# Optimization experiments

Measured on AMD Instinct MI355X. Metric: run time of the kernel, lower is better.

Reference implementation:

```python
import jax, jax.numpy as jnp
import numpy as np

N_NODES = 100000
NUM_ET = 8
IN_DIM = 128
N_EDGES = 100000


def setup_inputs() -> dict:
    key = jax.random.key(0)
    k1, k2, k3, k4 = jax.random.split(key, 4)
    z = jax.random.normal(k1, (N_NODES, IN_DIM), dtype=jnp.float32)
    # reset_parameters: normal with std = 1/sqrt(in_dim)
    weight = jax.random.normal(k2, (NUM_ET, IN_DIM), dtype=jnp.float32) / np.sqrt(IN_DIM)
    edge_src = jax.random.randint(k3, (NUM_ET, N_EDGES), 0, N_NODES, dtype=jnp.int64)
    edge_dst = jax.random.randint(k4, (NUM_ET, N_EDGES), 0, N_NODES, dtype=jnp.int64)
    return {"z": z, "weight": weight, "edge_src": edge_src, "edge_dst": edge_dst}


def reference(z, weight, edge_src, edge_dst):
    # For each edge type t and edge e: sigmoid( sum_d z[src,d] * z[dst,d] * weight[t,d] )
    zs = z[edge_src]                      # [T, E, D] gather
    zd = z[edge_dst]                      # [T, E, D] gather
    val = jnp.einsum('ted,ted,td->te', zs, zd, weight)  # [T, E]
    return jax.nn.sigmoid(val)
```

## Files before the change

kernel.cpp:

```cpp
#include <hip/hip_runtime.h>

typedef unsigned int   u32;
typedef unsigned short u16;

__device__ __forceinline__ u16 f2bf(float x) {
    u32 u = __builtin_bit_cast(u32, x);
    u = (u + 0x7fffu + ((u >> 16) & 1u)) >> 16;
    return (u16)u;
}
__device__ __forceinline__ float bf_lo(u32 q) { return __builtin_bit_cast(float, q << 16); }
__device__ __forceinline__ float bf_hi(u32 q) { return __builtin_bit_cast(float, q & 0xffff0000u); }

__global__ __launch_bounds__(256) void convert_z_kernel(
    const float* __restrict__ z, uint4* __restrict__ zb, int n8)
{
    int i = blockIdx.x * blockDim.x + threadIdx.x;
    const int stride = gridDim.x * blockDim.x;
    const float4* __restrict__ z4 = (const float4*)z;
    for (; i < n8; i += stride) {
        float4 a = z4[2 * i];
        float4 b = z4[2 * i + 1];
        u32 p0 = (u32)f2bf(a.x) | ((u32)f2bf(a.y) << 16);
        u32 p1 = (u32)f2bf(a.z) | ((u32)f2bf(a.w) << 16);
        u32 p2 = (u32)f2bf(b.x) | ((u32)f2bf(b.y) << 16);
        u32 p3 = (u32)f2bf(b.z) | ((u32)f2bf(b.w) << 16);
        zb[i] = make_uint4(p0, p1, p2, p3);
    }
}

__device__ __forceinline__ float dot8(const uint4& A, const uint4& B,
                                      const float4& w0, const float4& w1) {
    float p;
    p  = (bf_lo(A.x) * bf_lo(B.x)) * w0.x;
    p += (bf_hi(A.x) * bf_hi(B.x)) * w0.y;
    p += (bf_lo(A.y) * bf_lo(B.y)) * w0.z;
    p += (bf_hi(A.y) * bf_hi(B.y)) * w0.w;
    p += (bf_lo(A.z) * bf_lo(B.z)) * w1.x;
    p += (bf_hi(A.z) * bf_hi(B.z)) * w1.y;
    p += (bf_lo(A.w) * bf_lo(B.w)) * w1.z;
    p += (bf_hi(A.w) * bf_hi(B.w)) * w1.w;
    return p;
}

__device__ __forceinline__ float red16(float p) {
    p += __shfl_xor(p, 8);
    p += __shfl_xor(p, 4);
    p += __shfl_xor(p, 2);
    p += __shfl_xor(p, 1);
    return p;
}

__global__ __launch_bounds__(256) void mipd_bf16_u4_kernel(
    const uint4* __restrict__ zb,
    const float* __restrict__ weight,
    const int*   __restrict__ edge_src,
    const int*   __restrict__ edge_dst,
    float*       __restrict__ out,
    int E4)
{
    const int sub     = threadIdx.x & 15;
    const int gid     = (blockIdx.x * blockDim.x + threadIdx.x) >> 4;
    const int ngroups = (gridDim.x * blockDim.x) >> 4;
    const int t       = blockIdx.y;
    const int E       = E4 * 4;

    const float4* w4 = (const float4*)(weight + (size_t)t * 128 + sub * 8);
    const float4 w0 = w4[0], w1 = w4[1];

    const int4* src4 = (const int4*)(edge_src + (size_t)t * E);
    const int4* dst4 = (const int4*)(edge_dst + (size_t)t * E);
    float4*     out4 = (float4*)(out + (size_t)t * E);

    for (int b = gid; b < E4; b += ngroups) {
        const int4 S = src4[b];
        const int4 D = dst4[b];

        const uint4 A0 = zb[(size_t)S.x * 16 + sub];
        const uint4 B0 = zb[(size_t)D.x * 16 + sub];
        const uint4 A1 = zb[(size_t)S.y * 16 + sub];
        const uint4 B1 = zb[(size_t)D.y * 16 + sub];
        const uint4 A2 = zb[(size_t)S.z * 16 + sub];
        const uint4 B2 = zb[(size_t)D.z * 16 + sub];
        const uint4 A3 = zb[(size_t)S.w * 16 + sub];
        const uint4 B3 = zb[(size_t)D.w * 16 + sub];

        float p0 = red16(dot8(A0, B0, w0, w1));
        float p1 = red16(dot8(A1, B1, w0, w1));
        float p2 = red16(dot8(A2, B2, w0, w1));
        float p3 = red16(dot8(A3, B3, w0, w1));

        if (sub == 0) {
            float4 r;
            r.x = 1.0f / (1.0f + __expf(-p0));
            r.y = 1.0f / (1.0f + __expf(-p1));
            r.z = 1.0f / (1.0f + __expf(-p2));
            r.w = 1.0f / (1.0f + __expf(-p3));
            out4[b] = r;
        }
    }
}

__global__ __launch_bounds__(256) void mipd_bf16_kernel(
    const uint4* __restrict__ zb,
    const float* __restrict__ weight,
    const int*   __restrict__ edge_src,
    const int*   __restrict__ edge_dst,
    float*       __restrict__ out,
    int E)
{
    const int sub     = threadIdx.x & 15;
    const int gid     = (blockIdx.x * blockDim.x + threadIdx.x) >> 4;
    const int ngroups = (gridDim.x * blockDim.x) >> 4;
    const int t       = blockIdx.y;

    const float4* w4 = (const float4*)(weight + (size_t)t * 128 + sub * 8);
    const float4 w0 = w4[0], w1 = w4[1];

    const int* src_t = edge_src + (size_t)t * E;
    const int* dst_t = edge_dst + (size_t)t * E;
    float*     out_t = out      + (size_t)t * E;

    for (int e = gid; e < E; e += ngroups) {
        const uint4 A = zb[(size_t)src_t[e] * 16 + sub];
        const uint4 B = zb[(size_t)dst_t[e] * 16 + sub];
        float p = red16(dot8(A, B, w0, w1));
        if (sub == 0) out_t[e] = 1.0f / (1.0f + __expf(-p));
    }
}

__global__ __launch_bounds__(256) void mipd_f32_kernel(
    const float* __restrict__ z,
    const float* __restrict__ weight,
    const int*   __restrict__ edge_src,
    const int*   __restrict__ edge_dst,
    float*       __restrict__ out,
    int E)
{
    const int lane    = threadIdx.x & 31;
    const int gid     = (blockIdx.x * blockDim.x + threadIdx.x) >> 5;
    const int ngroups = (gridDim.x * blockDim.x) >> 5;
    const int t       = blockIdx.y;

    const float4* __restrict__ z4 = (const float4*)z;
    const float4  w = ((const float4*)weight)[t * 32 + lane];

    const int* src_t = edge_src + (size_t)t * E;
    const int* dst_t = edge_dst + (size_t)t * E;
    float*     out_t = out      + (size_t)t * E;

    for (int e = gid; e < E; e += ngroups) {
        const float4 a = z4[(size_t)src_t[e] * 32 + lane];
        const float4 b = z4[(size_t)dst_t[e] * 32 + lane];
        float p = a.x * b.x * w.x + a.y * b.y * w.y
                + a.z * b.z * w.z + a.w * b.w * w.w;
        p += __shfl_xor(p, 16);
        p += __shfl_xor(p, 8);
        p += __shfl_xor(p, 4);
        p += __shfl_xor(p, 2);
        p += __shfl_xor(p, 1);
        if (lane == 0) out_t[e] = 1.0f / (1.0f + __expf(-p));
    }
}

extern "C" void kernel_launch(void* const* d_in, const int* in_sizes, int n_in,
                              void* d_out, int out_size, void* d_ws, size_t ws_size,
                              hipStream_t stream) {
    const float* z      = (const float*)d_in[0];
    const float* weight = (const float*)d_in[1];
    const int*   e_src  = (const int*)d_in[2];
    const int*   e_dst  = (const int*)d_in[3];
    float*       out    = (float*)d_out;

    const int IN_DIM = 128;
    const int T = in_sizes[1] / IN_DIM;
    const int E = in_sizes[2] / T;
    const int N = in_sizes[0] / IN_DIM;

    const size_t zb_bytes = (size_t)N * IN_DIM * 2;

    if (ws_size >= zb_bytes) {
        uint4* zb = (uint4*)d_ws;
        const int n8 = N * IN_DIM / 8;
        hipLaunchKernelGGL(convert_z_kernel, dim3(2048), dim3(256), 0, stream,
                           z, zb, n8);
        if ((E & 3) == 0) {
            hipLaunchKernelGGL(mipd_bf16_u4_kernel, dim3(256, T), dim3(256), 0, stream,
                               zb, weight, e_src, e_dst, out, E >> 2);
        } else {
            hipLaunchKernelGGL(mipd_bf16_kernel, dim3(256, T), dim3(256), 0, stream,
                               zb, weight, e_src, e_dst, out, E);
        }
    } else {
        hipLaunchKernelGGL(mipd_f32_kernel, dim3(512, T), dim3(256), 0, stream,
                           z, weight, e_src, e_dst, out, E);
    }
}
```

Baseline: 68.17 us.

## Split bf16 feature rows into two halves and compute dot product in two passes

The bf16 copy of z is stored as two separate 64-dim halves. The dot product then runs in two kernel passes, one per half. The first pass writes partial sums to a workspace buffer, and the second adds its own half and applies the sigmoid. The aim is to shrink the gathered working set per pass so random row gathers hit cache more often. In exchange it reads the edge indices twice, adds a partial-sum write and read, and adds an extra kernel launch.

```diff
diff --git a/kernel.cpp b/kernel.cpp
--- a/kernel.cpp
+++ b/kernel.cpp
@@ -10,23 +10,6 @@
 }
 __device__ __forceinline__ float bf_lo(u32 q) { return __builtin_bit_cast(float, q << 16); }
 __device__ __forceinline__ float bf_hi(u32 q) { return __builtin_bit_cast(float, q & 0xffff0000u); }
-
-__global__ __launch_bounds__(256) void convert_z_kernel(
-    const float* __restrict__ z, uint4* __restrict__ zb, int n8)
-{
-    int i = blockIdx.x * blockDim.x + threadIdx.x;
-    const int stride = gridDim.x * blockDim.x;
-    const float4* __restrict__ z4 = (const float4*)z;
-    for (; i < n8; i += stride) {
-        float4 a = z4[2 * i];
-        float4 b = z4[2 * i + 1];
-        u32 p0 = (u32)f2bf(a.x) | ((u32)f2bf(a.y) << 16);
-        u32 p1 = (u32)f2bf(a.z) | ((u32)f2bf(a.w) << 16);
-        u32 p2 = (u32)f2bf(b.x) | ((u32)f2bf(b.y) << 16);
-        u32 p3 = (u32)f2bf(b.z) | ((u32)f2bf(b.w) << 16);
-        zb[i] = make_uint4(p0, p1, p2, p3);
-    }
-}
 
 __device__ __forceinline__ float dot8(const uint4& A, const uint4& B,
                                       const float4& w0, const float4& w1) {
@@ -42,12 +25,111 @@
     return p;
 }
 
-__device__ __forceinline__ float red16(float p) {
-    p += __shfl_xor(p, 8);
+__device__ __forceinline__ float red8(float p) {
     p += __shfl_xor(p, 4);
     p += __shfl_xor(p, 2);
     p += __shfl_xor(p, 1);
     return p;
+}
+__device__ __forceinline__ float red16(float p) {
+    p += __shfl_xor(p, 8);
+    return red8(p);
+}
+
+__global__ __launch_bounds__(256) void convert_z_split_kernel(
+    const float* __restrict__ z, uint4* __restrict__ zbL, uint4* __restrict__ zbH,
+    int n16)
+{
+    int i = blockIdx.x * blockDim.x + threadIdx.x;
+    const int stride = gridDim.x * blockDim.x;
+    const float4* __restrict__ z4 = (const float4*)z;
+    for (; i < n16; i += stride) {
+        float4 a = z4[2 * i];
+        float4 b = z4[2 * i + 1];
+        u32 p0 = (u32)f2bf(a.x) | ((u32)f2bf(a.y) << 16);
+        u32 p1 = (u32)f2bf(a.z) | ((u32)f2bf(a.w) << 16);
+        u32 p2 = (u32)f2bf(b.x) | ((u32)f2bf(b.y) << 16);
+        u32 p3 = (u32)f2bf(b.z) | ((u32)f2bf(b.w) << 16);
+        const int r = i >> 4;
+        const int j = i & 15;
+        if (j < 8) zbL[r * 8 + j]       = make_uint4(p0, p1, p2, p3);
+        else       zbH[r * 8 + (j - 8)] = make_uint4(p0, p1, p2, p3);
+    }
+}
+
+template <int PASS>
+__global__ __launch_bounds__(256) void mipd_half_kernel(
+    const uint4* __restrict__ zh,
+    const float* __restrict__ weight,
+    const int*   __restrict__ edge_src,
+    const int*   __restrict__ edge_dst,
+    float*       __restrict__ part,
+    float*       __restrict__ out,
+    int E4)
+{
+    const int sub     = threadIdx.x & 7;
+    const int gid     = (blockIdx.x * blockDim.x + threadIdx.x) >> 3;
+    const int ngroups = (gridDim.x * blockDim.x) >> 3;
+    const int t       = blockIdx.y;
+    const int E       = E4 * 4;
+
+    const float4* w4 = (const float4*)(weight + (size_t)t * 128 + PASS * 64 + sub * 8);
+    const float4 w0 = w4[0], w1 = w4[1];
+
+    const int4* src4 = (const int4*)(edge_src + (size_t)t * E);
+    const int4* dst4 = (const int4*)(edge_dst + (size_t)t * E);
+    float4*     par4 = (float4*)(part + (size_t)t * E);
+    float4*     out4 = (float4*)(out + (size_t)t * E);
+
+    for (int b = gid; b < E4; b += ngroups) {
+        const int4 S = src4[b];
+        const int4 D = dst4[b];
+
+        const uint4 A0 = zh[(size_t)S.x * 8 + sub];
+        const uint4 B0 = zh[(size_t)D.x * 8 + sub];
+        const uint4 A1 = zh[(size_t)S.y * 8 + sub];
+        const uint4 B1 = zh[(size_t)D.y * 8 + sub];
+        const uint4 A2 = zh[(size_t)S.z * 8 + sub];
+        const uint4 B2 = zh[(size_t)D.z * 8 + sub];
+        const uint4 A3 = zh[(size_t)S.w * 8 + sub];
+        const uint4 B3 = zh[(size_t)D.w * 8 + sub];
+
+        float p0 = red8(dot8(A0, B0, w0, w1));
+        float p1 = red8(dot8(A1, B1, w0, w1));
+        float p2 = red8(dot8(A2, B2, w0, w1));
+        float p3 = red8(dot8(A3, B3, w0, w1));
+
+        if (sub == 0) {
+            if (PASS == 0) {
+                par4[b] = make_float4(p0, p1, p2, p3);
+            } else {
+                const float4 q = par4[b];
+                float4 r;
+                r.x = 1.0f / (1.0f + __expf(-(p0 + q.x)));
+                r.y = 1.0f / (1.0f + __expf(-(p1 + q.y)));
+                r.z = 1.0f / (1.0f + __expf(-(p2 + q.z)));
+                r.w = 1.0f / (1.0f + __expf(-(p3 + q.w)));
+                out4[b] = r;
+            }
+        }
+    }
+}
+
+__global__ __launch_bounds__(256) void convert_z_kernel(
+    const float* __restrict__ z, uint4* __restrict__ zb, int n8)
+{
+    int i = blockIdx.x * blockDim.x + threadIdx.x;
+    const int stride = gridDim.x * blockDim.x;
+    const float4* __restrict__ z4 = (const float4*)z;
+    for (; i < n8; i += stride) {
+        float4 a = z4[2 * i];
+        float4 b = z4[2 * i + 1];
+        u32 p0 = (u32)f2bf(a.x) | ((u32)f2bf(a.y) << 16);
+        u32 p1 = (u32)f2bf(a.z) | ((u32)f2bf(a.w) << 16);
+        u32 p2 = (u32)f2bf(b.x) | ((u32)f2bf(b.y) << 16);
+        u32 p3 = (u32)f2bf(b.z) | ((u32)f2bf(b.w) << 16);
+        zb[i] = make_uint4(p0, p1, p2, p3);
+    }
 }
 
 __global__ __launch_bounds__(256) void mipd_bf16_u4_kernel(
@@ -74,7 +156,6 @@
     for (int b = gid; b < E4; b += ngroups) {
         const int4 S = src4[b];
         const int4 D = dst4[b];
-
         const uint4 A0 = zb[(size_t)S.x * 16 + sub];
         const uint4 B0 = zb[(size_t)D.x * 16 + sub];
         const uint4 A1 = zb[(size_t)S.y * 16 + sub];
@@ -97,34 +178,6 @@
             r.w = 1.0f / (1.0f + __expf(-p3));
             out4[b] = r;
         }
-    }
-}
-
-__global__ __launch_bounds__(256) void mipd_bf16_kernel(
-    const uint4* __restrict__ zb,
-    const float* __restrict__ weight,
-    const int*   __restrict__ edge_src,
-    const int*   __restrict__ edge_dst,
-    float*       __restrict__ out,
-    int E)
-{
-    const int sub     = threadIdx.x & 15;
-    const int gid     = (blockIdx.x * blockDim.x + threadIdx.x) >> 4;
-    const int ngroups = (gridDim.x * blockDim.x) >> 4;
-    const int t       = blockIdx.y;
-
-    const float4* w4 = (const float4*)(weight + (size_t)t * 128 + sub * 8);
-    const float4 w0 = w4[0], w1 = w4[1];
-
-    const int* src_t = edge_src + (size_t)t * E;
-    const int* dst_t = edge_dst + (size_t)t * E;
-    float*     out_t = out      + (size_t)t * E;
-
-    for (int e = gid; e < E; e += ngroups) {
-        const uint4 A = zb[(size_t)src_t[e] * 16 + sub];
-        const uint4 B = zb[(size_t)dst_t[e] * 16 + sub];
-        float p = red16(dot8(A, B, w0, w1));
-        if (sub == 0) out_t[e] = 1.0f / (1.0f + __expf(-p));
     }
 }
 
@@ -176,20 +229,28 @@
     const int E = in_sizes[2] / T;
     const int N = in_sizes[0] / IN_DIM;
 
-    const size_t zb_bytes = (size_t)N * IN_DIM * 2;
-
-    if (ws_size >= zb_bytes) {
+    const size_t half_bytes  = (size_t)N * 64 * 2;
+    const size_t part_bytes  = (size_t)T * E * 4;
+    const size_t split_need  = 2 * half_bytes + part_bytes;
+    const size_t single_need = (size_t)N * IN_DIM * 2;
+
+    if (ws_size >= split_need && (E & 3) == 0) {
+        uint4* zbL  = (uint4*)d_ws;
+        uint4* zbH  = zbL + (size_t)N * 8;
+        float* part = (float*)(zbH + (size_t)N * 8);
+        const int n16 = N * 16;
+        hipLaunchKernelGGL(convert_z_split_kernel, dim3(2048), dim3(256), 0, stream,
+                           z, zbL, zbH, n16);
+        hipLaunchKernelGGL((mipd_half_kernel<0>), dim3(256, T), dim3(256), 0, stream,
+                           zbL, weight, e_src, e_dst, part, out, E >> 2);
+        hipLaunchKernelGGL((mipd_half_kernel<1>), dim3(256, T), dim3(256), 0, stream,
+                           zbH, weight, e_src, e_dst, part, out, E >> 2);
+    } else if (ws_size >= single_need && (E & 3) == 0) {
         uint4* zb = (uint4*)d_ws;
-        const int n8 = N * IN_DIM / 8;
         hipLaunchKernelGGL(convert_z_kernel, dim3(2048), dim3(256), 0, stream,
-                           z, zb, n8);
-        if ((E & 3) == 0) {
-            hipLaunchKernelGGL(mipd_bf16_u4_kernel, dim3(256, T), dim3(256), 0, stream,
-                               zb, weight, e_src, e_dst, out, E >> 2);
-        } else {
-            hipLaunchKernelGGL(mipd_bf16_kernel, dim3(256, T), dim3(256), 0, stream,
-                               zb, weight, e_src, e_dst, out, E);
-        }
+                           z, zb, N * IN_DIM / 8);
+        hipLaunchKernelGGL(mipd_bf16_u4_kernel, dim3(256, T), dim3(256), 0, stream,
+                           zb, weight, e_src, e_dst, out, E >> 2);
     } else {
         hipLaunchKernelGGL(mipd_f32_kernel, dim3(512, T), dim3(256), 0, stream,
                            z, weight, e_src, e_dst, out, E);
```

New measurement: 66.15 us. 1.03x faster.

## Bin edges by source-node range to improve gather locality

Applied to the files above, without the earlier changes.

Adds histogram, scan and scatter kernels that bucket each edge type's edges into eight source-node ranges, packing src, dst and edge index into 64-bit records. The main kernel then processes one bucket per block group so source-row gathers stay within a small slice of the bf16 node table, and uses nontemporal loads and stores for streaming data. This aims to cut cache misses on random gathers but adds three extra launches, a single-block scan, extra traffic for the binned array, and scattered output writes.

```diff
diff --git a/kernel.cpp b/kernel.cpp
--- a/kernel.cpp
+++ b/kernel.cpp
@@ -1,7 +1,10 @@
 #include <hip/hip_runtime.h>
 
-typedef unsigned int   u32;
-typedef unsigned short u16;
+typedef unsigned int       u32;
+typedef unsigned short     u16;
+typedef unsigned long long u64;
+typedef __attribute__((ext_vector_type(4))) u32 u32x4;
+
 
 __device__ __forceinline__ u16 f2bf(float x) {
     u32 u = __builtin_bit_cast(u32, x);
@@ -10,23 +13,6 @@
 }
 __device__ __forceinline__ float bf_lo(u32 q) { return __builtin_bit_cast(float, q << 16); }
 __device__ __forceinline__ float bf_hi(u32 q) { return __builtin_bit_cast(float, q & 0xffff0000u); }
-
-__global__ __launch_bounds__(256) void convert_z_kernel(
-    const float* __restrict__ z, uint4* __restrict__ zb, int n8)
-{
-    int i = blockIdx.x * blockDim.x + threadIdx.x;
-    const int stride = gridDim.x * blockDim.x;
-    const float4* __restrict__ z4 = (const float4*)z;
-    for (; i < n8; i += stride) {
-        float4 a = z4[2 * i];
-        float4 b = z4[2 * i + 1];
-        u32 p0 = (u32)f2bf(a.x) | ((u32)f2bf(a.y) << 16);
-        u32 p1 = (u32)f2bf(a.z) | ((u32)f2bf(a.w) << 16);
-        u32 p2 = (u32)f2bf(b.x) | ((u32)f2bf(b.y) << 16);
-        u32 p3 = (u32)f2bf(b.z) | ((u32)f2bf(b.w) << 16);
-        zb[i] = make_uint4(p0, p1, p2, p3);
-    }
-}
 
 __device__ __forceinline__ float dot8(const uint4& A, const uint4& B,
                                       const float4& w0, const float4& w1) {
@@ -50,6 +36,166 @@
     return p;
 }
 
+__device__ __forceinline__ uint4 ld_nt16(const uint4* p) {
+    u32x4 v = __builtin_nontemporal_load((const u32x4*)p);
+    return make_uint4(v.x, v.y, v.z, v.w);
+}
+
+__device__ __forceinline__ float sigmoidf(float x) {
+    return 1.0f / (1.0f + __expf(-x));
+}
+
+__global__ __launch_bounds__(256) void convert_z_kernel(
+    const float* __restrict__ z, uint4* __restrict__ zb, int n8)
+{
+    int i = blockIdx.x * blockDim.x + threadIdx.x;
+    const int stride = gridDim.x * blockDim.x;
+    const float4* __restrict__ z4 = (const float4*)z;
+    for (; i < n8; i += stride) {
+        float4 a = z4[2 * i];
+        float4 b = z4[2 * i + 1];
+        u32 p0 = (u32)f2bf(a.x) | ((u32)f2bf(a.y) << 16);
+        u32 p1 = (u32)f2bf(a.z) | ((u32)f2bf(a.w) << 16);
+        u32 p2 = (u32)f2bf(b.x) | ((u32)f2bf(b.y) << 16);
+        u32 p3 = (u32)f2bf(b.z) | ((u32)f2bf(b.w) << 16);
+        zb[i] = make_uint4(p0, p1, p2, p3);
+    }
+}
+
+#define NBLKX 64
+#define NBT   (8 * NBLKX)
+#define NENT  (64 * NBT)
+#define NPT   (NENT / 1024)
+
+__global__ __launch_bounds__(256) void hist_kernel(
+    const int* __restrict__ edge_src, int E, int N,
+    u32* __restrict__ hist)
+{
+    __shared__ u32 h[64];
+    if (threadIdx.x < 64) h[threadIdx.x] = 0;
+    __syncthreads();
+    const int t = blockIdx.y;
+    const int B = t * NBLKX + blockIdx.x;
+    const int chunk = (E + NBLKX - 1) / NBLKX;
+    const int e0 = blockIdx.x * chunk;
+    const int e1 = min(E, e0 + chunk);
+    const float sc = 8.0f / (float)N;
+    const int* src = edge_src + (size_t)t * E;
+    for (int e = e0 + threadIdx.x; e < e1; e += 256) {
+        int s = src[e];
+        int sh = min(7, (int)((float)s * sc));
+        atomicAdd(&h[t * 8 + sh], 1u);
+    }
+    __syncthreads();
+    if (threadIdx.x < 64) hist[(u32)threadIdx.x * NBT + B] = h[threadIdx.x];
+}
+
+__global__ __launch_bounds__(1024) void scan_kernel(u32* __restrict__ hist)
+{
+    __shared__ u32 partial[1024];
+    const int tid = threadIdx.x;
+    u32 v[NPT];
+    u32 sum = 0;
+#pragma unroll
+    for (int j = 0; j < NPT; j++) { v[j] = hist[tid * NPT + j]; sum += v[j]; }
+    partial[tid] = sum;
+    __syncthreads();
+    for (int off = 1; off < 1024; off <<= 1) {
+        u32 x = (tid >= off) ? partial[tid - off] : 0u;
+        __syncthreads();
+        partial[tid] += x;
+        __syncthreads();
+    }
+    u32 base = (tid > 0) ? partial[tid - 1] : 0u;
+#pragma unroll
+    for (int j = 0; j < NPT; j++) { u32 x = v[j]; hist[tid * NPT + j] = base; base += x; }
+}
+
+__global__ __launch_bounds__(256) void scatter_kernel(
+    const int* __restrict__ edge_src, const int* __restrict__ edge_dst,
+    int E, int N, const u32* __restrict__ hist,
+    u64* __restrict__ binned)
+{
+    __shared__ u32 pos[64];
+    const int t = blockIdx.y;
+    const int B = t * NBLKX + blockIdx.x;
+    if (threadIdx.x < 64) pos[threadIdx.x] = hist[(u32)threadIdx.x * NBT + B];
+    __syncthreads();
+    const int chunk = (E + NBLKX - 1) / NBLKX;
+    const int e0 = blockIdx.x * chunk;
+    const int e1 = min(E, e0 + chunk);
+    const float sc = 8.0f / (float)N;
+    const int* src = edge_src + (size_t)t * E;
+    const int* dst = edge_dst + (size_t)t * E;
+    for (int e = e0 + threadIdx.x; e < e1; e += 256) {
+        int s = src[e];
+        int d = dst[e];
+        int sh = min(7, (int)((float)s * sc));
+        u32 p = atomicAdd(&pos[t * 8 + sh], 1u);
+        binned[p] = (u64)(u32)s | ((u64)(u32)d << 17) | ((u64)(u32)e << 34);
+    }
+}
+
+__global__ __launch_bounds__(256) void mipd_binned_kernel(
+    const uint4* __restrict__ zb,
+    const float* __restrict__ weight,
+    const u64*   __restrict__ binned,
+    const u32*   __restrict__ hist,
+    float*       __restrict__ out,
+    int E)
+{
+    const int t      = blockIdx.y;
+    const int shard  = blockIdx.x & 7;
+    const int bucket = t * 8 + shard;
+    const u32 start  = hist[(u32)bucket * NBT];
+    const u32 end    = (bucket == 63) ? (u32)(8 * E) : hist[(u32)(bucket + 1) * NBT];
+
+    const int sub  = threadIdx.x & 15;
+    const int rank = blockIdx.x >> 3;
+    const int g    = rank * 16 + (threadIdx.x >> 4);
+    const int ng   = (gridDim.x >> 3) * 16;
+
+    const float4* w4 = (const float4*)(weight + (size_t)t * 128 + sub * 8);
+    const float4 w0 = w4[0], w1 = w4[1];
+    float* out_t = out + (size_t)t * E;
+
+    const u32 nq = (end - start + 3) >> 2;
+    for (u32 q = g; q < nq; q += ng) {
+        const u32 b0 = start + q * 4;
+        const u64 p0 = __builtin_nontemporal_load(&binned[b0]);
+        const bool v1 = b0 + 1 < end, v2 = b0 + 2 < end, v3 = b0 + 3 < end;
+        const u64 p1 = v1 ? __builtin_nontemporal_load(&binned[b0 + 1]) : p0;
+        const u64 p2 = v2 ? __builtin_nontemporal_load(&binned[b0 + 2]) : p0;
+        const u64 p3 = v3 ? __builtin_nontemporal_load(&binned[b0 + 3]) : p0;
+
+        const u32 s0 = (u32)p0 & 0x1ffffu, d0 = (u32)(p0 >> 17) & 0x1ffffu, e0 = (u32)(p0 >> 34) & 0x1ffffu;
+        const u32 s1 = (u32)p1 & 0x1ffffu, d1 = (u32)(p1 >> 17) & 0x1ffffu, e1 = (u32)(p1 >> 34) & 0x1ffffu;
+        const u32 s2 = (u32)p2 & 0x1ffffu, d2 = (u32)(p2 >> 17) & 0x1ffffu, e2 = (u32)(p2 >> 34) & 0x1ffffu;
+        const u32 s3 = (u32)p3 & 0x1ffffu, d3 = (u32)(p3 >> 17) & 0x1ffffu, e3 = (u32)(p3 >> 34) & 0x1ffffu;
+
+        const uint4 A0 = zb[(size_t)s0 * 16 + sub];
+        const uint4 A1 = zb[(size_t)s1 * 16 + sub];
+        const uint4 A2 = zb[(size_t)s2 * 16 + sub];
+        const uint4 A3 = zb[(size_t)s3 * 16 + sub];
+        const uint4 B0 = ld_nt16(&zb[(size_t)d0 * 16 + sub]);
+        const uint4 B1 = ld_nt16(&zb[(size_t)d1 * 16 + sub]);
+        const uint4 B2 = ld_nt16(&zb[(size_t)d2 * 16 + sub]);
+        const uint4 B3 = ld_nt16(&zb[(size_t)d3 * 16 + sub]);
+
+        float r0 = red16(dot8(A0, B0, w0, w1));
+        float r1 = red16(dot8(A1, B1, w0, w1));
+        float r2 = red16(dot8(A2, B2, w0, w1));
+        float r3 = red16(dot8(A3, B3, w0, w1));
+
+        if (sub == 0) {
+            __builtin_nontemporal_store(sigmoidf(r0), &out_t[e0]);
+            if (v1) __builtin_nontemporal_store(sigmoidf(r1), &out_t[e1]);
+            if (v2) __builtin_nontemporal_store(sigmoidf(r2), &out_t[e2]);
+            if (v3) __builtin_nontemporal_store(sigmoidf(r3), &out_t[e3]);
+        }
+    }
+}
+
 __global__ __launch_bounds__(256) void mipd_bf16_u4_kernel(
     const uint4* __restrict__ zb,
     const float* __restrict__ weight,
@@ -74,7 +220,6 @@
     for (int b = gid; b < E4; b += ngroups) {
         const int4 S = src4[b];
         const int4 D = dst4[b];
-
         const uint4 A0 = zb[(size_t)S.x * 16 + sub];
         const uint4 B0 = zb[(size_t)D.x * 16 + sub];
         const uint4 A1 = zb[(size_t)S.y * 16 + sub];
@@ -91,40 +236,12 @@
 
         if (sub == 0) {
             float4 r;
-            r.x = 1.0f / (1.0f + __expf(-p0));
-            r.y = 1.0f / (1.0f + __expf(-p1));
-            r.z = 1.0f / (1.0f + __expf(-p2));
-            r.w = 1.0f / (1.0f + __expf(-p3));
+            r.x = sigmoidf(p0);
+            r.y = sigmoidf(p1);
+            r.z = sigmoidf(p2);
+            r.w = sigmoidf(p3);
             out4[b] = r;
         }
-    }
-}
-
-__global__ __launch_bounds__(256) void mipd_bf16_kernel(
-    const uint4* __restrict__ zb,
-    const float* __restrict__ weight,
-    const int*   __restrict__ edge_src,
-    const int*   __restrict__ edge_dst,
-    float*       __restrict__ out,
-    int E)
-{
-    const int sub     = threadIdx.x & 15;
-    const int gid     = (blockIdx.x * blockDim.x + threadIdx.x) >> 4;
-    const int ngroups = (gridDim.x * blockDim.x) >> 4;
-    const int t       = blockIdx.y;
-
-    const float4* w4 = (const float4*)(weight + (size_t)t * 128 + sub * 8);
-    const float4 w0 = w4[0], w1 = w4[1];
-
-    const int* src_t = edge_src + (size_t)t * E;
-    const int* dst_t = edge_dst + (size_t)t * E;
-    float*     out_t = out      + (size_t)t * E;
-
-    for (int e = gid; e < E; e += ngroups) {
-        const uint4 A = zb[(size_t)src_t[e] * 16 + sub];
-        const uint4 B = zb[(size_t)dst_t[e] * 16 + sub];
-        float p = red16(dot8(A, B, w0, w1));
-        if (sub == 0) out_t[e] = 1.0f / (1.0f + __expf(-p));
     }
 }
 
@@ -158,7 +275,7 @@
         p += __shfl_xor(p, 4);
         p += __shfl_xor(p, 2);
         p += __shfl_xor(p, 1);
-        if (lane == 0) out_t[e] = 1.0f / (1.0f + __expf(-p));
+        if (lane == 0) out_t[e] = sigmoidf(p);
     }
 }
 
@@ -176,20 +293,34 @@
     const int E = in_sizes[2] / T;
     const int N = in_sizes[0] / IN_DIM;
 
-    const size_t zb_bytes = (size_t)N * IN_DIM * 2;
-
-    if (ws_size >= zb_bytes) {
+    const size_t zb_bytes     = (size_t)N * IN_DIM * 2;
+    const size_t binned_bytes = (size_t)T * E * 8;
+    const size_t hist_bytes   = (size_t)NENT * 4;
+    const size_t fast_need    = zb_bytes + binned_bytes + hist_bytes;
+
+    const bool fast = (T == 8) && (N < 131072) && (E < 131072) &&
+                      (ws_size >= fast_need);
+
+    if (fast) {
+        uint4* zb     = (uint4*)d_ws;
+        u64*   binned = (u64*)((char*)d_ws + zb_bytes);
+        u32*   hist   = (u32*)((char*)d_ws + zb_bytes + binned_bytes);
+
+        hipLaunchKernelGGL(convert_z_kernel, dim3(2048), dim3(256), 0, stream,
+                           z, zb, N * IN_DIM / 8);
+        hipLaunchKernelGGL(hist_kernel, dim3(NBLKX, 8), dim3(256), 0, stream,
+                           e_src, E, N, hist);
+        hipLaunchKernelGGL(scan_kernel, dim3(1), dim3(1024), 0, stream, hist);
+        hipLaunchKernelGGL(scatter_kernel, dim3(NBLKX, 8), dim3(256), 0, stream,
+                           e_src, e_dst, E, N, hist, binned);
+        hipLaunchKernelGGL(mipd_binned_kernel, dim3(256, 8), dim3(256), 0, stream,
+                           zb, weight, binned, hist, out, E);
+    } else if (ws_size >= zb_bytes && (E & 3) == 0) {
         uint4* zb = (uint4*)d_ws;
-        const int n8 = N * IN_DIM / 8;
         hipLaunchKernelGGL(convert_z_kernel, dim3(2048), dim3(256), 0, stream,
-                           z, zb, n8);
-        if ((E & 3) == 0) {
-            hipLaunchKernelGGL(mipd_bf16_u4_kernel, dim3(256, T), dim3(256), 0, stream,
-                               zb, weight, e_src, e_dst, out, E >> 2);
-        } else {
-            hipLaunchKernelGGL(mipd_bf16_kernel, dim3(256, T), dim3(256), 0, stream,
-                               zb, weight, e_src, e_dst, out, E);
-        }
+                           z, zb, N * IN_DIM / 8);
+        hipLaunchKernelGGL(mipd_bf16_u4_kernel, dim3(256, T), dim3(256), 0, stream,
+                           zb, weight, e_src, e_dst, out, E >> 2);
     } else {
         hipLaunchKernelGGL(mipd_f32_kernel, dim3(512, T), dim3(256), 0, stream,
                            z, weight, e_src, e_dst, out, E);
```

Result: slower. 109.9 us (+61.3%).

## Split feature dim into 8 slices for cache-resident gathers plus reduction pass

Applied to the files above, without the earlier changes.

Converts z to bf16 in a slice-major layout, so each of 8 feature slices (16 dims, 32 bytes per node) forms a contiguous 3.2MB table. A gather kernel assigns each block one slice and one edge type, with two lanes per edge, and writes bf16 partial dot products to a workspace. A third kernel sums the 8 partials and applies the sigmoid. The aim is to keep each slice's table resident in L2 for its random gathers, at the cost of an extra kernel, extra partial-sum traffic, and bf16 rounding of partial sums.

```diff
diff --git a/kernel.cpp b/kernel.cpp
--- a/kernel.cpp
+++ b/kernel.cpp
@@ -1,7 +1,8 @@
 #include <hip/hip_runtime.h>
 
-typedef unsigned int   u32;
-typedef unsigned short u16;
+typedef unsigned int       u32;
+typedef unsigned short     u16;
+
 
 __device__ __forceinline__ u16 f2bf(float x) {
     u32 u = __builtin_bit_cast(u32, x);
@@ -10,23 +11,6 @@
 }
 __device__ __forceinline__ float bf_lo(u32 q) { return __builtin_bit_cast(float, q << 16); }
 __device__ __forceinline__ float bf_hi(u32 q) { return __builtin_bit_cast(float, q & 0xffff0000u); }
-
-__global__ __launch_bounds__(256) void convert_z_kernel(
-    const float* __restrict__ z, uint4* __restrict__ zb, int n8)
-{
-    int i = blockIdx.x * blockDim.x + threadIdx.x;
-    const int stride = gridDim.x * blockDim.x;
-    const float4* __restrict__ z4 = (const float4*)z;
-    for (; i < n8; i += stride) {
-        float4 a = z4[2 * i];
-        float4 b = z4[2 * i + 1];
-        u32 p0 = (u32)f2bf(a.x) | ((u32)f2bf(a.y) << 16);
-        u32 p1 = (u32)f2bf(a.z) | ((u32)f2bf(a.w) << 16);
-        u32 p2 = (u32)f2bf(b.x) | ((u32)f2bf(b.y) << 16);
-        u32 p3 = (u32)f2bf(b.z) | ((u32)f2bf(b.w) << 16);
-        zb[i] = make_uint4(p0, p1, p2, p3);
-    }
-}
 
 __device__ __forceinline__ float dot8(const uint4& A, const uint4& B,
                                       const float4& w0, const float4& w1) {
@@ -42,12 +26,129 @@
     return p;
 }
 
+__device__ __forceinline__ float sigmoidf(float x) {
+    return 1.0f / (1.0f + __expf(-x));
+}
+
 __device__ __forceinline__ float red16(float p) {
     p += __shfl_xor(p, 8);
     p += __shfl_xor(p, 4);
     p += __shfl_xor(p, 2);
     p += __shfl_xor(p, 1);
     return p;
+}
+
+
+__global__ __launch_bounds__(256) void convert_slice_kernel(
+    const float* __restrict__ z, uint4* __restrict__ sl, int N)
+{
+    int i = blockIdx.x * blockDim.x + threadIdx.x;
+    const int stride = gridDim.x * blockDim.x;
+    const int total = N * 8;
+    for (; i < total; i += stride) {
+        const int node = i >> 3;
+        const int k    = i & 7;
+        const float4* zp = (const float4*)(z + (size_t)node * 128 + k * 16);
+        float4 a = zp[0], b = zp[1], c = zp[2], d = zp[3];
+        uint4 lo, hi;
+        lo.x = (u32)f2bf(a.x) | ((u32)f2bf(a.y) << 16);
+        lo.y = (u32)f2bf(a.z) | ((u32)f2bf(a.w) << 16);
+        lo.z = (u32)f2bf(b.x) | ((u32)f2bf(b.y) << 16);
+        lo.w = (u32)f2bf(b.z) | ((u32)f2bf(b.w) << 16);
+        hi.x = (u32)f2bf(c.x) | ((u32)f2bf(c.y) << 16);
+        hi.y = (u32)f2bf(c.z) | ((u32)f2bf(c.w) << 16);
+        hi.z = (u32)f2bf(d.x) | ((u32)f2bf(d.y) << 16);
+        hi.w = (u32)f2bf(d.z) | ((u32)f2bf(d.w) << 16);
+        uint4* dst = sl + ((size_t)k * N + node) * 2;
+        dst[0] = lo;
+        dst[1] = hi;
+    }
+}
+
+__global__ __launch_bounds__(256) void gather_slice_kernel(
+    const uint4* __restrict__ sl,
+    const float* __restrict__ weight,
+    const int*   __restrict__ edge_src,
+    const int*   __restrict__ edge_dst,
+    u16*         __restrict__ part,
+    int E, int N, int TE)
+{
+    const int k    = blockIdx.x & 7;
+    const int t    = blockIdx.y;
+    const int half = threadIdx.x & 1;
+    const int pair  = (blockIdx.x >> 3) * 128 + (threadIdx.x >> 1);
+    const int npair = (gridDim.x >> 3) * 128;
+
+    const float4* wb = (const float4*)(weight + (size_t)t * 128 + k * 16 + half * 8);
+    const float4 w0 = wb[0], w1 = wb[1];
+
+    const int* src = edge_src + (size_t)t * E;
+    const int* dst = edge_dst + (size_t)t * E;
+    u16* part_tk = part + (size_t)k * TE + (size_t)t * E;
+    const uint4* slk = sl + (size_t)k * N * 2;
+
+    for (int e = pair * 2; e < E; e += npair * 2) {
+        const int s0 = src[e],     d0 = dst[e];
+        const int s1 = src[e + 1], d1 = dst[e + 1];
+
+        const uint4 A0 = slk[(size_t)s0 * 2 + half];
+        const uint4 B0 = slk[(size_t)d0 * 2 + half];
+        const uint4 A1 = slk[(size_t)s1 * 2 + half];
+        const uint4 B1 = slk[(size_t)d1 * 2 + half];
+
+        float p0 = dot8(A0, B0, w0, w1);
+        float p1 = dot8(A1, B1, w0, w1);
+        p0 += __shfl_xor(p0, 1);
+        p1 += __shfl_xor(p1, 1);
+
+        if (half == 0) {
+            *(u32*)(part_tk + e) = (u32)f2bf(p0) | ((u32)f2bf(p1) << 16);
+        }
+    }
+}
+
+__global__ __launch_bounds__(256) void reduce_slice_kernel(
+    const u16* __restrict__ part, float* __restrict__ out, int TE)
+{
+    int i = blockIdx.x * blockDim.x + threadIdx.x;
+    const int stride = gridDim.x * blockDim.x;
+    const int n8 = TE / 8;
+    float4* out4 = (float4*)out;
+    for (; i < n8; i += stride) {
+        float acc[8] = {0, 0, 0, 0, 0, 0, 0, 0};
+#pragma unroll
+        for (int k = 0; k < 8; k++) {
+            const uint4 v = *(const uint4*)(part + (size_t)k * TE + (size_t)i * 8);
+            acc[0] += bf_lo(v.x); acc[1] += bf_hi(v.x);
+            acc[2] += bf_lo(v.y); acc[3] += bf_hi(v.y);
+            acc[4] += bf_lo(v.z); acc[5] += bf_hi(v.z);
+            acc[6] += bf_lo(v.w); acc[7] += bf_hi(v.w);
+        }
+        float4 o0, o1;
+        o0.x = sigmoidf(acc[0]); o0.y = sigmoidf(acc[1]);
+        o0.z = sigmoidf(acc[2]); o0.w = sigmoidf(acc[3]);
+        o1.x = sigmoidf(acc[4]); o1.y = sigmoidf(acc[5]);
+        o1.z = sigmoidf(acc[6]); o1.w = sigmoidf(acc[7]);
+        out4[(size_t)i * 2]     = o0;
+        out4[(size_t)i * 2 + 1] = o1;
+    }
+}
+
+__global__ __launch_bounds__(256) void convert_z_kernel(
+    const float* __restrict__ z, uint4* __restrict__ zb, int n8)
+{
+    int i = blockIdx.x * blockDim.x + threadIdx.x;
+    const int stride = gridDim.x * blockDim.x;
+    const float4* __restrict__ z4 = (const float4*)z;
+    for (; i < n8; i += stride) {
+        float4 a = z4[2 * i];
+        float4 b = z4[2 * i + 1];
+        u32 p0 = (u32)f2bf(a.x) | ((u32)f2bf(a.y) << 16);
+        u32 p1 = (u32)f2bf(a.z) | ((u32)f2bf(a.w) << 16);
+        u32 p2 = (u32)f2bf(b.x) | ((u32)f2bf(b.y) << 16);
+        u32 p3 = (u32)f2bf(b.z) | ((u32)f2bf(b.w) << 16);
+        zb[i] = make_uint4(p0, p1, p2, p3);
+    }
 }
 
 __global__ __launch_bounds__(256) void mipd_bf16_u4_kernel(
@@ -74,7 +175,6 @@
     for (int b = gid; b < E4; b += ngroups) {
         const int4 S = src4[b];
         const int4 D = dst4[b];
-
         const uint4 A0 = zb[(size_t)S.x * 16 + sub];
         const uint4 B0 = zb[(size_t)D.x * 16 + sub];
         const uint4 A1 = zb[(size_t)S.y * 16 + sub];
@@ -91,40 +191,12 @@
 
         if (sub == 0) {
             float4 r;
-            r.x = 1.0f / (1.0f + __expf(-p0));
-            r.y = 1.0f / (1.0f + __expf(-p1));
-            r.z = 1.0f / (1.0f + __expf(-p2));
-            r.w = 1.0f / (1.0f + __expf(-p3));
+            r.x = sigmoidf(p0);
+            r.y = sigmoidf(p1);
+            r.z = sigmoidf(p2);
+            r.w = sigmoidf(p3);
             out4[b] = r;
         }
-    }
-}
-
-__global__ __launch_bounds__(256) void mipd_bf16_kernel(
-    const uint4* __restrict__ zb,
-    const float* __restrict__ weight,
-    const int*   __restrict__ edge_src,
-    const int*   __restrict__ edge_dst,
-    float*       __restrict__ out,
-    int E)
-{
-    const int sub     = threadIdx.x & 15;
-    const int gid     = (blockIdx.x * blockDim.x + threadIdx.x) >> 4;
-    const int ngroups = (gridDim.x * blockDim.x) >> 4;
-    const int t       = blockIdx.y;
-
-    const float4* w4 = (const float4*)(weight + (size_t)t * 128 + sub * 8);
-    const float4 w0 = w4[0], w1 = w4[1];
-
-    const int* src_t = edge_src + (size_t)t * E;
-    const int* dst_t = edge_dst + (size_t)t * E;
-    float*     out_t = out      + (size_t)t * E;
-
-    for (int e = gid; e < E; e += ngroups) {
-        const uint4 A = zb[(size_t)src_t[e] * 16 + sub];
-        const uint4 B = zb[(size_t)dst_t[e] * 16 + sub];
-        float p = red16(dot8(A, B, w0, w1));
-        if (sub == 0) out_t[e] = 1.0f / (1.0f + __expf(-p));
     }
 }
 
@@ -158,7 +230,7 @@
         p += __shfl_xor(p, 4);
         p += __shfl_xor(p, 2);
         p += __shfl_xor(p, 1);
-        if (lane == 0) out_t[e] = 1.0f / (1.0f + __expf(-p));
+        if (lane == 0) out_t[e] = sigmoidf(p);
     }
 }
 
@@ -175,21 +247,31 @@
     const int T = in_sizes[1] / IN_DIM;
     const int E = in_sizes[2] / T;
     const int N = in_sizes[0] / IN_DIM;
-
-    const size_t zb_bytes = (size_t)N * IN_DIM * 2;
-
-    if (ws_size >= zb_bytes) {
+    const int TE = T * E;
+
+    const size_t sl_bytes   = (size_t)N * IN_DIM * 2;
+    const size_t part_bytes = (size_t)TE * 8 * 2;
+    const size_t slice_need = sl_bytes + part_bytes;
+
+    const bool slice_ok = (in_sizes[1] % IN_DIM == 0) && (in_sizes[0] % IN_DIM == 0) &&
+                          (E % 8 == 0) && (ws_size >= slice_need);
+
+    if (slice_ok) {
+        uint4* sl   = (uint4*)d_ws;
+        u16*   part = (u16*)((char*)d_ws + sl_bytes);
+
+        hipLaunchKernelGGL(convert_slice_kernel, dim3(2048), dim3(256), 0, stream,
+                           z, sl, N);
+        hipLaunchKernelGGL(gather_slice_kernel, dim3(256, T), dim3(256), 0, stream,
+                           sl, weight, e_src, e_dst, part, E, N, TE);
+        hipLaunchKernelGGL(reduce_slice_kernel, dim3(512), dim3(256), 0, stream,
+                           part, out, TE);
+    } else if (ws_size >= sl_bytes && (E & 3) == 0) {
         uint4* zb = (uint4*)d_ws;
-        const int n8 = N * IN_DIM / 8;
         hipLaunchKernelGGL(convert_z_kernel, dim3(2048), dim3(256), 0, stream,
-                           z, zb, n8);
-        if ((E & 3) == 0) {
-            hipLaunchKernelGGL(mipd_bf16_u4_kernel, dim3(256, T), dim3(256), 0, stream,
-                               zb, weight, e_src, e_dst, out, E >> 2);
-        } else {
-            hipLaunchKernelGGL(mipd_bf16_kernel, dim3(256, T), dim3(256), 0, stream,
-                               zb, weight, e_src, e_dst, out, E);
-        }
+                           z, zb, N * IN_DIM / 8);
+        hipLaunchKernelGGL(mipd_bf16_u4_kernel, dim3(256, T), dim3(256), 0, stream,
+                           zb, weight, e_src, e_dst, out, E >> 2);
     } else {
         hipLaunchKernelGGL(mipd_f32_kernel, dim3(512, T), dim3(256), 0, stream,
                            z, weight, e_src, e_dst, out, E);
```

New measurement: 85.75 us. 25.8% more time.
